# Optimization experiments

Hardware: AMD Instinct MI355X
Metric: run time of the kernel (lower is better)

## Reference

```python
import jax, jax.numpy as jnp
import numpy as np

K = 16          # filter order (number of Laplacian powers)
MLP_OUT = 16    # mlp_hid == mlp_out for mlp_nlayers == 1
D_PE = 64       # phi output dim
BN_EPS = 1e-5
B, N, M = 8, 1024, 128
E = 131072


def setup_inputs() -> dict:
    key = jax.random.key(0)
    ks = jax.random.split(key, 12)
    # Symmetric, spectrally-bounded Laplacian surrogate so 15 matrix powers stay finite.
    A = jax.random.normal(ks[0], (B, N, N), dtype=jnp.float32)
    Lap = (A + jnp.swapaxes(A, -1, -2)) * (0.5 / jnp.sqrt(jnp.float32(N)))
    W = jax.random.normal(ks[1], (B, N, M), dtype=jnp.float32)
    edge_index = jax.random.randint(ks[2], (2, E), 0, B * N, dtype=jnp.int64)
    batch = jnp.repeat(jnp.arange(B, dtype=jnp.int64), N)
    # MLP layer (k -> MLP_OUT) + BatchNorm affine params
    lin_w = jax.random.normal(ks[3], (K, MLP_OUT), dtype=jnp.float32) / jnp.sqrt(jnp.float32(K))
    lin_b = jnp.zeros((MLP_OUT,), dtype=jnp.float32)
    bn_gamma = jnp.ones((MLP_OUT,), dtype=jnp.float32)
    bn_beta = jnp.zeros((MLP_OUT,), dtype=jnp.float32)
    # phi: GIN-style 2-layer MLP after neighbor aggregation
    phi_w1 = jax.random.normal(ks[4], (MLP_OUT, D_PE), dtype=jnp.float32) / jnp.sqrt(jnp.float32(MLP_OUT))
    phi_b1 = jnp.zeros((D_PE,), dtype=jnp.float32)
    phi_w2 = jax.random.normal(ks[5], (D_PE, D_PE), dtype=jnp.float32) / jnp.sqrt(jnp.float32(D_PE))
    phi_b2 = jnp.zeros((D_PE,), dtype=jnp.float32)
    return {"Lap": Lap, "W": W, "lin_w": lin_w, "lin_b": lin_b,
            "bn_gamma": bn_gamma, "bn_beta": bn_beta,
            "phi_w1": phi_w1, "phi_b1": phi_b1, "phi_w2": phi_w2, "phi_b2": phi_b2,
            "edge_index": edge_index, "batch": batch}


def _filter(S, W0):
    """Sequential power filter: returns [k, N, M] = [W0, S@W0, S^2@W0, ...]."""
    def step(out, _):
        nxt = S @ out
        return nxt, nxt
    _, rest = jax.lax.scan(step, W0, None, length=K - 1)
    return jnp.concatenate([W0[None], rest], axis=0)


def reference(Lap, W, lin_w, lin_b, bn_gamma, bn_beta,
              phi_w1, phi_b1, phi_w2, phi_b2, edge_index, batch):
    # Batched filter over all graphs: [B, k, N, M] -> [B, N, M, k]
    feat = jax.vmap(_filter)(Lap, W)
    feat = jnp.transpose(feat, (0, 2, 3, 1))
    # Linear over k -> MLP_OUT channels: [B, N, M, C]
    h = feat @ lin_w + lin_b
    # BatchNorm1d (training mode), per-graph statistics over (N, M) per channel,
    # matching the torch per-graph loop where BN sees [M, C, N].
    mean = jnp.mean(h, axis=(1, 2), keepdims=True)
    var = jnp.var(h, axis=(1, 2), keepdims=True)
    h = (h - mean) * jax.lax.rsqrt(var + BN_EPS) * bn_gamma + bn_beta
    h = jax.nn.relu(h)
    # phi: pool random-sample dim M, flatten graphs -> [N_sum, C]
    x = jnp.mean(h, axis=2).reshape(-1, h.shape[-1])
    src, dst = edge_index[0], edge_index[1]
    agg = jax.ops.segment_sum(x[src], dst, num_segments=x.shape[0])
    g = x + agg  # GIN aggregation
    out = jax.nn.relu(g @ phi_w1 + phi_b1) @ phi_w2 + phi_b2  # [N_sum, D_PE]
    return out
```

## Files before the change

### kernel.cpp

```cpp
#include <hip/hip_runtime.h>

#define B 8
#define N 1024
#define M 128
#define KF 16
#define C 16
#define DPE 64
#define NE 131072
#define NV (B*N)
#define NM (N*M)
#define BN_EPS 1e-5f

typedef short bf16x8 __attribute__((ext_vector_type(8)));
typedef float f32x4 __attribute__((ext_vector_type(4)));

__device__ inline unsigned short f2bf_rne(float f) {
    unsigned u = __float_as_uint(f);
    u += 0x7fffu + ((u >> 16) & 1u);
    return (unsigned short)(u >> 16);
}
__device__ inline void split_bf16(float v, unsigned short& hi, unsigned short& lo) {
    hi = f2bf_rne(v);
    float hf = __uint_as_float((unsigned)hi << 16);
    lo = f2bf_rne(v - hf);
}
union U4 { uint4 v; unsigned short s[8]; };

__device__ __host__ inline size_t SF4(int b, int nsub, int ks, int hl, int l) {
    return ((((size_t)b * 64 + nsub) * 32 + ks) * 2 + hl) * 64 + l;
}
__device__ __host__ inline size_t PF4(int b, int msub, int ks, int hl, int l) {
    return ((((size_t)b * 8 + msub) * 32 + ks) * 2 + hl) * 64 + l;
}
#define PFBUF ((size_t)B * 8 * 32 * 2 * 64)

__global__ __launch_bounds__(256) void prep_s(const float* __restrict__ Lap, uint4* __restrict__ Sf) {
    int b = blockIdx.x & 7, nb = blockIdx.x >> 3;
    int t = threadIdx.x;
    int nl = t >> 4, kg = t & 15;
    int n = nb * 16 + nl;
    const float* row = Lap + ((size_t)b * N + n) * N;
    #pragma unroll
    for (int jj = 0; jj < 8; jj++) {
        int koct = kg + 16 * jj;
        int k0 = koct * 8;
        float4 f0 = *(const float4*)(row + k0);
        float4 f1 = *(const float4*)(row + k0 + 4);
        float e[8] = {f0.x, f0.y, f0.z, f0.w, f1.x, f1.y, f1.z, f1.w};
        U4 hi, lo;
        #pragma unroll
        for (int j = 0; j < 8; j++) split_bf16(e[j], hi.s[j], lo.s[j]);
        int ks = k0 >> 5;
        int lf = nl + 16 * (koct & 3);
        Sf[SF4(b, nb, ks, 0, lf)] = hi.v;
        Sf[SF4(b, nb, ks, 1, lf)] = lo.v;
    }
}

__global__ __launch_bounds__(256) void prep_w_plane(const float* __restrict__ W, float* __restrict__ feat) {
    __shared__ float T[32][33];
    int b = blockIdx.x & 7;
    int tile = blockIdx.x >> 3;
    int nt = tile & 31, mt = tile >> 5;
    int n0 = nt * 32, m0 = mt * 32;
    int t = threadIdx.x;
    {
        int nl = t >> 3, mq = t & 7;
        float4 v = *(const float4*)(W + ((size_t)b * N + n0 + nl) * M + m0 + mq * 4);
        T[nl][mq * 4 + 0] = v.x; T[nl][mq * 4 + 1] = v.y;
        T[nl][mq * 4 + 2] = v.z; T[nl][mq * 4 + 3] = v.w;
    }
    __syncthreads();
    {
        int ml = t >> 3, nq = t & 7;
        float4 v = make_float4(T[nq * 4 + 0][ml], T[nq * 4 + 1][ml], T[nq * 4 + 2][ml], T[nq * 4 + 3][ml]);
        float* plane = feat + (size_t)b * KF * NM;
        *(float4*)(plane + (size_t)(m0 + ml) * N + n0 + nq * 4) = v;
    }
}

__global__ __launch_bounds__(256) void prep_w_frag(const float* __restrict__ W, uint4* __restrict__ Pf) {
    int b = blockIdx.x & 7;
    int r = (blockIdx.x >> 3) * 256 + threadIdx.x;
    int msub = r >> 11, ks = (r >> 6) & 31, l = r & 63;
    int m = 16 * msub + (l & 15);
    U4 hi, lo;
    #pragma unroll
    for (int j = 0; j < 8; j++) {
        int n = 32 * ks + 8 * (l >> 4) + j;
        float v = W[((size_t)b * N + n) * M + m];
        split_bf16(v, hi.s[j], lo.s[j]);
    }
    Pf[PF4(b, msub, ks, 0, l)] = hi.v;
    Pf[PF4(b, msub, ks, 1, l)] = lo.v;
}

__global__ __launch_bounds__(512) void gemm_chain(const uint4* __restrict__ Sf,
                                                  uint4* __restrict__ PfA,
                                                  uint4* __restrict__ PfB,
                                                  float* __restrict__ feat,
                                                  unsigned* bar) {
    extern __shared__ __align__(16) char smem[];
    uint4* ldsS = (uint4*)smem;
    float* Dl = (float*)(smem + 131072);

    int b = blockIdx.x & 7, bx = blockIdx.x >> 3;
    int t = threadIdx.x;
    int w = t >> 6, lane = t & 63;
    size_t sbase = SF4(b, 2 * bx, 0, 0, 0);
    int n0 = 32 * bx;

    #pragma unroll
    for (int i = 0; i < 16; i++) ldsS[t + 512 * i] = Sf[sbase + t + 512 * i];
    __syncthreads();

    #pragma unroll 1
    for (int k = 0; k < KF - 1; k++) {
        const uint4* PfIn = (k & 1) ? PfB : PfA;
        uint4* PfOut      = (k & 1) ? PfA : PfB;
        const uint4* Pw = PfIn + (size_t)(b * 8 + w) * 4096;

        f32x4 acc0 = {}, acc1 = {};
        uint4 ah = Pw[lane], al = Pw[64 + lane];
        #pragma unroll 4
        for (int ks = 0; ks < 32; ks++) {
            uint4 nh, nl2;
            if (ks < 31) {
                nh  = Pw[(size_t)(ks + 1) * 128 + lane];
                nl2 = Pw[(size_t)(ks + 1) * 128 + 64 + lane];
            }
            bf16x8 b0h = __builtin_bit_cast(bf16x8, ldsS[ks * 128 + lane]);
            bf16x8 b0l = __builtin_bit_cast(bf16x8, ldsS[ks * 128 + 64 + lane]);
            bf16x8 b1h = __builtin_bit_cast(bf16x8, ldsS[4096 + ks * 128 + lane]);
            bf16x8 b1l = __builtin_bit_cast(bf16x8, ldsS[4096 + ks * 128 + 64 + lane]);
            bf16x8 Ah = __builtin_bit_cast(bf16x8, ah);
            bf16x8 Al = __builtin_bit_cast(bf16x8, al);
            acc0 = __builtin_amdgcn_mfma_f32_16x16x32_bf16(Ah, b0h, acc0, 0, 0, 0);
            acc0 = __builtin_amdgcn_mfma_f32_16x16x32_bf16(Ah, b0l, acc0, 0, 0, 0);
            acc0 = __builtin_amdgcn_mfma_f32_16x16x32_bf16(Al, b0h, acc0, 0, 0, 0);
            acc1 = __builtin_amdgcn_mfma_f32_16x16x32_bf16(Ah, b1h, acc1, 0, 0, 0);
            acc1 = __builtin_amdgcn_mfma_f32_16x16x32_bf16(Ah, b1l, acc1, 0, 0, 0);
            acc1 = __builtin_amdgcn_mfma_f32_16x16x32_bf16(Al, b1h, acc1, 0, 0, 0);
            ah = nh; al = nl2;
        }

        #pragma unroll
        for (int r = 0; r < 4; r++) {
            int m = 16 * w + 4 * (lane >> 4) + r;
            Dl[m * 36 + (lane & 15)] = acc0[r];
            Dl[m * 36 + 16 + (lane & 15)] = acc1[r];
        }
        __syncthreads();
        {
            int m = t >> 2, c0 = (t & 3) * 8;
            float* plane = feat + ((size_t)b * KF + (k + 1)) * NM + (size_t)m * N + n0 + c0;
            ((float4*)plane)[0] = *(const float4*)&Dl[m * 36 + c0];
            ((float4*)plane)[1] = *(const float4*)&Dl[m * 36 + c0 + 4];
        }
        if (k < KF - 2) {
            {
                int l = t & 63;
                int m = 16 * w + (l & 15);
                int ncol = 8 * (l >> 4);
                float4 v0 = *(const float4*)&Dl[m * 36 + ncol];
                float4 v1 = *(const float4*)&Dl[m * 36 + ncol + 4];
                float e[8] = {v0.x, v0.y, v0.z, v0.w, v1.x, v1.y, v1.z, v1.w};
                U4 hi, lo;
                #pragma unroll
                for (int j = 0; j < 8; j++) split_bf16(e[j], hi.s[j], lo.s[j]);
                PfOut[PF4(b, w, bx, 0, l)] = hi.v;
                PfOut[PF4(b, w, bx, 1, l)] = lo.v;
            }
            __syncthreads();
            if (t == 0) {
                __hip_atomic_fetch_add(&bar[b * 32], 1u, __ATOMIC_RELAXED,
                                       __HIP_MEMORY_SCOPE_AGENT);
                unsigned target = 32u * (unsigned)(k + 1);
                while (__hip_atomic_load(&bar[b * 32], __ATOMIC_RELAXED,
                                         __HIP_MEMORY_SCOPE_AGENT) < target)
                    __builtin_amdgcn_s_sleep(1);
            }
            __syncthreads();
            asm volatile("buffer_inv sc0\n\ts_waitcnt vmcnt(0)" ::: "memory");
        } else {
            __syncthreads();
        }
    }
}

__global__ __launch_bounds__(256) void bn_stats(const float* __restrict__ feat,
                                                const float* __restrict__ lin_w,
                                                const float* __restrict__ lin_b,
                                                float* __restrict__ stats) {
    __shared__ float wls[KF * C];
    __shared__ float red[4][2][C];
    int t = threadIdx.x;
    wls[t] = lin_w[t];
    __syncthreads();
    int b = blockIdx.x & 7;
    int i = (blockIdx.x >> 3) * 256 + t;
    const float4* fb = (const float4*)(feat + (size_t)b * KF * NM);

    float4 hacc[C];
    #pragma unroll
    for (int c = 0; c < C; c++) {
        float bb = lin_b[c];
        hacc[c] = make_float4(bb, bb, bb, bb);
    }
    for (int kk = 0; kk < KF; kk++) {
        float4 pv = fb[(size_t)kk * (NM / 4) + i];
        #pragma unroll
        for (int c = 0; c < C; c++) {
            float wv = wls[kk * C + c];
            hacc[c].x = fmaf(pv.x, wv, hacc[c].x);
            hacc[c].y = fmaf(pv.y, wv, hacc[c].y);
            hacc[c].z = fmaf(pv.z, wv, hacc[c].z);
            hacc[c].w = fmaf(pv.w, wv, hacc[c].w);
        }
    }
    float s[C], ss[C];
    #pragma unroll
    for (int c = 0; c < C; c++) {
        float4 h = hacc[c];
        s[c] = h.x + h.y + h.z + h.w;
        ss[c] = h.x * h.x + h.y * h.y + h.z * h.z + h.w * h.w;
    }
    #pragma unroll
    for (int off = 32; off > 0; off >>= 1)
        #pragma unroll
        for (int c = 0; c < C; c++) {
            s[c] += __shfl_down(s[c], off);
            ss[c] += __shfl_down(ss[c], off);
        }
    if ((t & 63) == 0) {
        int wv = t >> 6;
        #pragma unroll
        for (int c = 0; c < C; c++) { red[wv][0][c] = s[c]; red[wv][1][c] = ss[c]; }
    }
    __syncthreads();
    if (t < 32) {
        int which = t >> 4, c = t & 15;
        float v = red[0][which][c] + red[1][which][c] + red[2][which][c] + red[3][which][c];
        atomicAdd(&stats[b * 32 + which * 16 + c], v);
    }
}

__global__ __launch_bounds__(256) void bn_x(const float* __restrict__ feat,
                                            const float* __restrict__ lin_w,
                                            const float* __restrict__ lin_b,
                                            const float* __restrict__ gam,
                                            const float* __restrict__ bet,
                                            const float* __restrict__ stats,
                                            float* __restrict__ x) {
    __shared__ float wls[KF * C];
    __shared__ float red[8][32 * 17];
    int t = threadIdx.x;
    wls[t] = lin_w[t];
    __syncthreads();
    int grp = blockIdx.x;
    int b = grp & 7, n0 = (grp >> 3) * 32;
    int nl = t & 31, mg = t >> 5;
    int n = n0 + nl;

    const float inv_nm = 1.0f / (float)NM;
    float sc[C], sh[C], bb[C];
    #pragma unroll
    for (int c = 0; c < C; c++) {
        float mean = stats[b * 32 + c] * inv_nm;
        float var = stats[b * 32 + 16 + c] * inv_nm - mean * mean;
        sc[c] = gam[c] * rsqrtf(var + BN_EPS);
        sh[c] = bet[c] - mean * sc[c];
        bb[c] = lin_b[c];
    }
    const float* fb = feat + (size_t)b * KF * NM + n;
    float y[C] = {};
    for (int m = mg * 16; m < mg * 16 + 16; m++) {
        float p[KF];
        #pragma unroll
        for (int kk = 0; kk < KF; kk++) p[kk] = fb[(size_t)kk * NM + (size_t)m * N];
        #pragma unroll
        for (int c = 0; c < C; c++) {
            float h = bb[c];
            #pragma unroll
            for (int kk = 0; kk < KF; kk++) h = fmaf(p[kk], wls[kk * C + c], h);
            y[c] += fmaxf(fmaf(h, sc[c], sh[c]), 0.0f);
        }
    }
    #pragma unroll
    for (int c = 0; c < C; c++) red[mg][nl * 17 + c] = y[c];
    __syncthreads();
    #pragma unroll
    for (int q = 0; q < 2; q++) {
        int slot = t + q * 256;
        int snl = slot >> 4, c = slot & 15;
        float v = 0.0f;
        #pragma unroll
        for (int m8 = 0; m8 < 8; m8++) v += red[m8][snl * 17 + c];
        v *= (1.0f / (float)M);
        x[((size_t)b * N + n0 + snl) * C + c] = v;
    }
}

__global__ __launch_bounds__(256) void edge_hist(const int* __restrict__ ei, int* __restrict__ cnt) {
    int e = blockIdx.x * 256 + threadIdx.x;
    bool is64 = (ei[1] == 0 && ei[3] == 0 && ei[5] == 0 && ei[7] == 0);
    int dst = is64 ? ei[2 * (NE + e)] : ei[NE + e];
    atomicAdd(&cnt[dst], 1);
}

__global__ __launch_bounds__(256) void edge_scan(const int* __restrict__ cnt,
                                                 int* __restrict__ off, int* __restrict__ cur) {
    __shared__ int ss[256];
    int t = threadIdx.x;
    int base = t * 32;
    int local[32];
    int s = 0;
    #pragma unroll
    for (int i = 0; i < 32; i++) { local[i] = cnt[base + i]; s += local[i]; }
    ss[t] = s;
    __syncthreads();
    #pragma unroll
    for (int d = 1; d < 256; d <<= 1) {
        int v = (t >= d) ? ss[t - d] : 0;
        __syncthreads();
        ss[t] += v;
        __syncthreads();
    }
    int excl = ss[t] - s;
    #pragma unroll
    for (int i = 0; i < 32; i++) { off[base + i] = excl; cur[base + i] = excl; excl += local[i]; }
}

__global__ __launch_bounds__(256) void edge_fill(const int* __restrict__ ei,
                                                 int* __restrict__ cur, int* __restrict__ bucket) {
    int e = blockIdx.x * 256 + threadIdx.x;
    bool is64 = (ei[1] == 0 && ei[3] == 0 && ei[5] == 0 && ei[7] == 0);
    int src, dst;
    if (is64) { src = ei[2 * e]; dst = ei[2 * (NE + e)]; }
    else      { src = ei[e];     dst = ei[NE + e]; }
    int pos = atomicAdd(&cur[dst], 1);
    bucket[pos] = src;
}

__global__ __launch_bounds__(256) void edge_gather(const int* __restrict__ cnt,
                                                   const int* __restrict__ off,
                                                   const int* __restrict__ bucket,
                                                   const float* __restrict__ x,
                                                   float* __restrict__ g) {
    int t = threadIdx.x;
    int grp = t >> 4, c = t & 15;
    int n = blockIdx.x * 16 + grp;
    int o = off[n], d = cnt[n];
    float v = x[(size_t)n * C + c];
    int j = 0;
    for (; j + 4 <= d; j += 4) {
        int s0 = bucket[o + j], s1 = bucket[o + j + 1];
        int s2 = bucket[o + j + 2], s3 = bucket[o + j + 3];
        v += x[(size_t)s0 * C + c];
        v += x[(size_t)s1 * C + c];
        v += x[(size_t)s2 * C + c];
        v += x[(size_t)s3 * C + c];
    }
    for (; j < d; j++) v += x[(size_t)bucket[o + j] * C + c];
    g[(size_t)n * C + c] = v;
}

__global__ __launch_bounds__(256) void phi1_k(const float* __restrict__ g,
                                              const float* __restrict__ w1,
                                              const float* __restrict__ b1,
                                              float* __restrict__ h1) {
    __shared__ float w1s[C * DPE];
    __shared__ float gs[4 * C];
    int t = threadIdx.x;
    int row0 = blockIdx.x * 4;
    #pragma unroll
    for (int q = 0; q < 4; q++) w1s[t + q * 256] = w1[t + q * 256];
    if (t < 64) gs[t] = g[row0 * C + t];
    __syncthreads();
    int r = t >> 6, j = t & 63;
    float h = b1[j];
    #pragma unroll
    for (int c = 0; c < C; c++) h = fmaf(gs[r * C + c], w1s[c * DPE + j], h);
    h1[(row0 + r) * DPE + j] = fmaxf(h, 0.0f);
}

__global__ __launch_bounds__(256) void phi2_k(const float* __restrict__ h1,
                                              const float* __restrict__ w2,
                                              const float* __restrict__ b2,
                                              float* __restrict__ out) {
    __shared__ float w2s[DPE * DPE];
    __shared__ float hs[4 * DPE];
    int t = threadIdx.x;
    int row0 = blockIdx.x * 4;
    #pragma unroll
    for (int q = 0; q < 16; q++) w2s[t + q * 256] = w2[t + q * 256];
    hs[t] = h1[row0 * DPE + t];
    __syncthreads();
    int r = t >> 6, d = t & 63;
    float o = b2[d];
    #pragma unroll
    for (int j = 0; j < DPE; j++) o = fmaf(hs[r * DPE + j], w2s[j * DPE + d], o);
    out[(row0 + r) * DPE + d] = o;
}

extern "C" void kernel_launch(void* const* d_in, const int* in_sizes, int n_in,
                              void* d_out, int out_size, void* d_ws, size_t ws_size,
                              hipStream_t stream) {
    const float* Lap   = (const float*)d_in[0];
    const float* W     = (const float*)d_in[1];
    const float* lin_w = (const float*)d_in[2];
    const float* lin_b = (const float*)d_in[3];
    const float* gam   = (const float*)d_in[4];
    const float* bet   = (const float*)d_in[5];
    const float* w1    = (const float*)d_in[6];
    const float* b1    = (const float*)d_in[7];
    const float* w2    = (const float*)d_in[8];
    const float* b2    = (const float*)d_in[9];
    const int*   ei    = (const int*)d_in[10];

    char* wsb = (char*)d_ws;
    float* feat  = (float*)wsb;
    uint4* Sf    = (uint4*)(wsb + ((size_t)64 << 20));
    uint4* Pf    = (uint4*)(wsb + ((size_t)96 << 20));
    float* stats = (float*)(wsb + ((size_t)104 << 20));
    unsigned* bar = (unsigned*)(stats + 256);
    float* x     = stats + 2048;
    float* g     = x + (size_t)NV * C;
    float* h1    = g + (size_t)NV * C;
    int*   cnt   = (int*)(h1 + (size_t)NV * DPE);
    int*   off   = cnt + NV;
    int*   cur   = off + NV;
    int*   bucket= cur + NV;
    float* out   = (float*)d_out;

    static bool attr_set = false;
    if (!attr_set) {
        hipFuncSetAttribute((const void*)gemm_chain,
                            hipFuncAttributeMaxDynamicSharedMemorySize, 149504);
        attr_set = true;
    }

    hipMemsetAsync(stats, 0, 8192, stream);
    hipMemsetAsync(cnt, 0, NV * sizeof(int), stream);
    prep_s<<<dim3(512), 256, 0, stream>>>(Lap, Sf);
    prep_w_plane<<<dim3(1024), 256, 0, stream>>>(W, feat);
    prep_w_frag<<<dim3(512), 256, 0, stream>>>(W, Pf);
    gemm_chain<<<dim3(256), 512, 149504, stream>>>(Sf, Pf, Pf + PFBUF, feat, bar);
    bn_stats<<<dim3(1024), 256, 0, stream>>>(feat, lin_w, lin_b, stats);
    bn_x<<<dim3(256), 256, 0, stream>>>(feat, lin_w, lin_b, gam, bet, stats, x);
    edge_hist<<<dim3(NE / 256), 256, 0, stream>>>(ei, cnt);
    edge_scan<<<dim3(1), 256, 0, stream>>>(cnt, off, cur);
    edge_fill<<<dim3(NE / 256), 256, 0, stream>>>(ei, cur, bucket);
    edge_gather<<<dim3(NV / 16), 256, 0, stream>>>(cnt, off, bucket, x, g);
    phi1_k<<<dim3(2048), 256, 0, stream>>>(g, w1, b1, h1);
    phi2_k<<<dim3(2048), 256, 0, stream>>>(h1, w2, b2, out);
}
```

Baseline: 333.2 us.

## Fuse edge gather and phi MLP into one kernel; deepen A-fragment prefetch

The edge gather, phi layer 1 and phi layer 2 kernels are merged into one kernel that keeps the aggregated features and hidden activations in shared memory. This removes two launches and the global round-trips for g and h1. Separately, the GEMM chain inner loop now prefetches A fragments four k-steps ahead with a register ring instead of one step ahead, to hide global load latency at the cost of more registers. Each fused block also reloads the full w2 matrix for only 16 nodes.

```diff
diff --git a/kernel.cpp b/kernel.cpp
--- a/kernel.cpp
+++ b/kernel.cpp
@@ -121,27 +121,31 @@
         const uint4* Pw = PfIn + (size_t)(b * 8 + w) * 4096;
 
         f32x4 acc0 = {}, acc1 = {};
-        uint4 ah = Pw[lane], al = Pw[64 + lane];
+        uint4 ph[4], pl[4];
+        #pragma unroll
+        for (int q = 0; q < 4; q++) {
+            ph[q] = Pw[(size_t)q * 128 + lane];
+            pl[q] = Pw[(size_t)q * 128 + 64 + lane];
+        }
         #pragma unroll 4
         for (int ks = 0; ks < 32; ks++) {
-            uint4 nh, nl2;
-            if (ks < 31) {
-                nh  = Pw[(size_t)(ks + 1) * 128 + lane];
-                nl2 = Pw[(size_t)(ks + 1) * 128 + 64 + lane];
+            uint4 ahu = ph[ks & 3], alu = pl[ks & 3];
+            if (ks < 28) {
+                ph[ks & 3] = Pw[(size_t)(ks + 4) * 128 + lane];
+                pl[ks & 3] = Pw[(size_t)(ks + 4) * 128 + 64 + lane];
             }
             bf16x8 b0h = __builtin_bit_cast(bf16x8, ldsS[ks * 128 + lane]);
             bf16x8 b0l = __builtin_bit_cast(bf16x8, ldsS[ks * 128 + 64 + lane]);
             bf16x8 b1h = __builtin_bit_cast(bf16x8, ldsS[4096 + ks * 128 + lane]);
             bf16x8 b1l = __builtin_bit_cast(bf16x8, ldsS[4096 + ks * 128 + 64 + lane]);
-            bf16x8 Ah = __builtin_bit_cast(bf16x8, ah);
-            bf16x8 Al = __builtin_bit_cast(bf16x8, al);
+            bf16x8 Ah = __builtin_bit_cast(bf16x8, ahu);
+            bf16x8 Al = __builtin_bit_cast(bf16x8, alu);
             acc0 = __builtin_amdgcn_mfma_f32_16x16x32_bf16(Ah, b0h, acc0, 0, 0, 0);
             acc0 = __builtin_amdgcn_mfma_f32_16x16x32_bf16(Ah, b0l, acc0, 0, 0, 0);
             acc0 = __builtin_amdgcn_mfma_f32_16x16x32_bf16(Al, b0h, acc0, 0, 0, 0);
             acc1 = __builtin_amdgcn_mfma_f32_16x16x32_bf16(Ah, b1h, acc1, 0, 0, 0);
             acc1 = __builtin_amdgcn_mfma_f32_16x16x32_bf16(Ah, b1l, acc1, 0, 0, 0);
             acc1 = __builtin_amdgcn_mfma_f32_16x16x32_bf16(Al, b1h, acc1, 0, 0, 0);
-            ah = nh; al = nl2;
         }
 
         #pragma unroll
@@ -342,65 +346,64 @@
     bucket[pos] = src;
 }
 
-__global__ __launch_bounds__(256) void edge_gather(const int* __restrict__ cnt,
-                                                   const int* __restrict__ off,
-                                                   const int* __restrict__ bucket,
-                                                   const float* __restrict__ x,
-                                                   float* __restrict__ g) {
-    int t = threadIdx.x;
-    int grp = t >> 4, c = t & 15;
-    int n = blockIdx.x * 16 + grp;
-    int o = off[n], d = cnt[n];
-    float v = x[(size_t)n * C + c];
-    int j = 0;
-    for (; j + 4 <= d; j += 4) {
-        int s0 = bucket[o + j], s1 = bucket[o + j + 1];
-        int s2 = bucket[o + j + 2], s3 = bucket[o + j + 3];
-        v += x[(size_t)s0 * C + c];
-        v += x[(size_t)s1 * C + c];
-        v += x[(size_t)s2 * C + c];
-        v += x[(size_t)s3 * C + c];
-    }
-    for (; j < d; j++) v += x[(size_t)bucket[o + j] * C + c];
-    g[(size_t)n * C + c] = v;
-}
-
-__global__ __launch_bounds__(256) void phi1_k(const float* __restrict__ g,
-                                              const float* __restrict__ w1,
-                                              const float* __restrict__ b1,
-                                              float* __restrict__ h1) {
+__global__ __launch_bounds__(256) void phi_fused(const int* __restrict__ cnt,
+                                                 const int* __restrict__ off,
+                                                 const int* __restrict__ bucket,
+                                                 const float* __restrict__ x,
+                                                 const float* __restrict__ w1,
+                                                 const float* __restrict__ b1,
+                                                 const float* __restrict__ w2,
+                                                 const float* __restrict__ b2,
+                                                 float* __restrict__ out) {
     __shared__ float w1s[C * DPE];
-    __shared__ float gs[4 * C];
-    int t = threadIdx.x;
-    int row0 = blockIdx.x * 4;
+    __shared__ float w2s[DPE * DPE];
+    __shared__ float b2s[DPE];
+    __shared__ float gsh[16][17];
+    __shared__ float h1sh[16][DPE];
+    int t = threadIdx.x;
     #pragma unroll
     for (int q = 0; q < 4; q++) w1s[t + q * 256] = w1[t + q * 256];
-    if (t < 64) gs[t] = g[row0 * C + t];
-    __syncthreads();
-    int r = t >> 6, j = t & 63;
-    float h = b1[j];
-    #pragma unroll
-    for (int c = 0; c < C; c++) h = fmaf(gs[r * C + c], w1s[c * DPE + j], h);
-    h1[(row0 + r) * DPE + j] = fmaxf(h, 0.0f);
-}
-
-__global__ __launch_bounds__(256) void phi2_k(const float* __restrict__ h1,
-                                              const float* __restrict__ w2,
-                                              const float* __restrict__ b2,
-                                              float* __restrict__ out) {
-    __shared__ float w2s[DPE * DPE];
-    __shared__ float hs[4 * DPE];
-    int t = threadIdx.x;
-    int row0 = blockIdx.x * 4;
     #pragma unroll
     for (int q = 0; q < 16; q++) w2s[t + q * 256] = w2[t + q * 256];
-    hs[t] = h1[row0 * DPE + t];
-    __syncthreads();
-    int r = t >> 6, d = t & 63;
-    float o = b2[d];
-    #pragma unroll
-    for (int j = 0; j < DPE; j++) o = fmaf(hs[r * DPE + j], w2s[j * DPE + d], o);
-    out[(row0 + r) * DPE + d] = o;
+    if (t < DPE) b2s[t] = b2[t];
+
+    {
+        int nl = t >> 4, c = t & 15;
+        int n = blockIdx.x * 16 + nl;
+        int o = off[n], d = cnt[n];
+        float v = x[(size_t)n * C + c];
+        int j = 0;
+        for (; j + 4 <= d; j += 4) {
+            int s0 = bucket[o + j], s1 = bucket[o + j + 1];
+            int s2 = bucket[o + j + 2], s3 = bucket[o + j + 3];
+            v += x[(size_t)s0 * C + c];
+            v += x[(size_t)s1 * C + c];
+            v += x[(size_t)s2 * C + c];
+            v += x[(size_t)s3 * C + c];
+        }
+        for (; j < d; j++) v += x[(size_t)bucket[o + j] * C + c];
+        gsh[nl][c] = v;
+    }
+    __syncthreads();
+    #pragma unroll
+    for (int q = 0; q < 4; q++) {
+        int item = t + 256 * q;
+        int node = item >> 6, j = item & 63;
+        float h = b1[j];
+        #pragma unroll
+        for (int c = 0; c < C; c++) h = fmaf(gsh[node][c], w1s[c * DPE + j], h);
+        h1sh[node][j] = fmaxf(h, 0.0f);
+    }
+    __syncthreads();
+    #pragma unroll
+    for (int q = 0; q < 4; q++) {
+        int item = t + 256 * q;
+        int node = item >> 6, d = item & 63;
+        float o2 = b2s[d];
+        #pragma unroll
+        for (int j = 0; j < DPE; j++) o2 = fmaf(h1sh[node][j], w2s[j * DPE + d], o2);
+        out[((size_t)blockIdx.x * 16 + node) * DPE + d] = o2;
+    }
 }
 
 extern "C" void kernel_launch(void* const* d_in, const int* in_sizes, int n_in,
@@ -425,9 +428,7 @@
     float* stats = (float*)(wsb + ((size_t)104 << 20));
     unsigned* bar = (unsigned*)(stats + 256);
     float* x     = stats + 2048;
-    float* g     = x + (size_t)NV * C;
-    float* h1    = g + (size_t)NV * C;
-    int*   cnt   = (int*)(h1 + (size_t)NV * DPE);
+    int*   cnt   = (int*)(x + (size_t)NV * C);
     int*   off   = cnt + NV;
     int*   cur   = off + NV;
     int*   bucket= cur + NV;
@@ -451,7 +452,5 @@
     edge_hist<<<dim3(NE / 256), 256, 0, stream>>>(ei, cnt);
     edge_scan<<<dim3(1), 256, 0, stream>>>(cnt, off, cur);
     edge_fill<<<dim3(NE / 256), 256, 0, stream>>>(ei, cur, bucket);
-    edge_gather<<<dim3(NV / 16), 256, 0, stream>>>(cnt, off, bucket, x, g);
-    phi1_k<<<dim3(2048), 256, 0, stream>>>(g, w1, b1, h1);
-    phi2_k<<<dim3(2048), 256, 0, stream>>>(h1, w2, b2, out);
-}
+    phi_fused<<<dim3(NV / 16), 256, 0, stream>>>(cnt, off, bucket, x, w1, b1, w2, b2, out);
+}
```

New measurement: 317.7 us. 4.7% less time.
